# Performance work log

Hardware: AMD Instinct MI355X
Metric: run time of the kernel (lower is better)

Reference implementation:

```python
import jax, jax.numpy as jnp
import numpy as np

CENTER_LR = 0.5  # EMA learning rate for centers (init arg lr)


def setup_inputs() -> dict:
    key = jax.random.key(0)
    k1, k2, k3 = jax.random.split(key, 3)
    B, D, C = 131072, 256, 1000
    feats = jax.random.normal(k1, (B, D), dtype=jnp.float32)
    centers = jax.random.normal(k2, (C, D), dtype=jnp.float32)
    labels = jax.random.randint(k3, (B,), 0, C, dtype=jnp.int64)
    return {"feats": feats, "centers": centers, "labels": labels}


def reference(feats, centers, labels):
    # EMA center update (done under no_grad in the original):
    # for each class c present in the batch:
    #   centers[c] = (1-lr)*centers[c] + lr*mean(feats[labels==c])
    C = centers.shape[0]
    counts = jax.ops.segment_sum(jnp.ones(labels.shape, feats.dtype), labels,
                                 num_segments=C)                       # [C]
    sums = jax.ops.segment_sum(feats, labels, num_segments=C)          # [C, D]
    means = sums / jnp.maximum(counts, 1.0)[:, None]                   # [C, D]
    present = (counts > 0)[:, None]
    new_centers = jnp.where(present,
                            (1.0 - CENTER_LR) * centers + CENTER_LR * means,
                            centers)                                   # [C, D]
    new_centers = jax.lax.stop_gradient(new_centers)
    # loss = 0.5 * mean_i ||f_i - c_{y_i}||^2
    sel = new_centers[labels]                                          # [B, D]
    diff = feats - sel
    loss = 0.5 * jnp.mean(jnp.sum(diff * diff, axis=1))
    return loss
```

## Files before the change

kernel.cpp:

```cpp
#include <hip/hip_runtime.h>


#define DDIM 256
#define DDIM4 64
#define CHUNK 2048

__global__ __launch_bounds__(1024) void k0_zero(int* __restrict__ counts,
                                                float* __restrict__ scalars) {
    int t = threadIdx.x;
    counts[t] = 0;
    if (t < 4) scalars[t] = 0.f;
}

__global__ __launch_bounds__(256) void k1_hist(const int* __restrict__ labels,
                                               int* __restrict__ counts,
                                               int B, int C) {
    __shared__ int h[1024];
    for (int i = threadIdx.x; i < 1024; i += 256) h[i] = 0;
    __syncthreads();
    int stride = gridDim.x * 256;
    for (int i = blockIdx.x * 256 + threadIdx.x; i < B; i += stride)
        atomicAdd(&h[labels[i]], 1);
    __syncthreads();
    for (int i = threadIdx.x; i < C; i += 256) {
        int v = h[i];
        if (v) atomicAdd(&counts[i], v);
    }
}

__global__ __launch_bounds__(1024) void k2_scan(const int* __restrict__ counts,
                                                int* __restrict__ offsets,
                                                int* __restrict__ cursor, int C) {
    __shared__ int sc[1024];
    int t = threadIdx.x;
    int mine = (t < C) ? counts[t] : 0;
    sc[t] = mine;
    __syncthreads();
    for (int off = 1; off < 1024; off <<= 1) {
        int add = (t >= off) ? sc[t - off] : 0;
        __syncthreads();
        sc[t] += add;
        __syncthreads();
    }
    if (t < C) {
        int e = sc[t] - mine;
        offsets[t] = e;
        cursor[t]  = e;
    }
}

__global__ __launch_bounds__(256) void k3_scatter(const int* __restrict__ labels,
                                                  int* __restrict__ cursor,
                                                  int* __restrict__ rowidx, int B) {
    int stride = gridDim.x * 256;
    for (int i = blockIdx.x * 256 + threadIdx.x; i < B; i += stride) {
        int c = labels[i];
        int pos = atomicAdd(&cursor[c], 1);
        rowidx[pos] = i;
    }
}

__global__ __launch_bounds__(256) void k4_class(const float4* __restrict__ feats4,
                                                const float* __restrict__ centers,
                                                const int* __restrict__ rowidx,
                                                const int* __restrict__ counts,
                                                const int* __restrict__ offsets,
                                                float* __restrict__ scalars) {
    __shared__ int rows[CHUNK];
    __shared__ float comb[4 * DDIM];
    __shared__ float red[12];

    int c = blockIdx.x;
    int count = counts[c];
    int start = offsets[c];
    int t = threadIdx.x;
    int wave = t >> 6, lane = t & 63;

    float4 acc = make_float4(0.f, 0.f, 0.f, 0.f);
    float ff = 0.f;

    for (int cs = 0; cs < count; cs += CHUNK) {
        int n = min(CHUNK, count - cs);
        for (int i = t; i < n; i += 256) rows[i] = rowidx[start + cs + i];
        __syncthreads();
        int r = wave;
        for (; r + 12 < n; r += 16) {
            int r0 = rows[r], r1 = rows[r + 4], r2 = rows[r + 8], r3 = rows[r + 12];
            float4 v0 = feats4[r0 * DDIM4 + lane];
            float4 v1 = feats4[r1 * DDIM4 + lane];
            float4 v2 = feats4[r2 * DDIM4 + lane];
            float4 v3 = feats4[r3 * DDIM4 + lane];
            acc.x += v0.x; acc.y += v0.y; acc.z += v0.z; acc.w += v0.w;
            ff += v0.x*v0.x + v0.y*v0.y + v0.z*v0.z + v0.w*v0.w;
            acc.x += v1.x; acc.y += v1.y; acc.z += v1.z; acc.w += v1.w;
            ff += v1.x*v1.x + v1.y*v1.y + v1.z*v1.z + v1.w*v1.w;
            acc.x += v2.x; acc.y += v2.y; acc.z += v2.z; acc.w += v2.w;
            ff += v2.x*v2.x + v2.y*v2.y + v2.z*v2.z + v2.w*v2.w;
            acc.x += v3.x; acc.y += v3.y; acc.z += v3.z; acc.w += v3.w;
            ff += v3.x*v3.x + v3.y*v3.y + v3.z*v3.z + v3.w*v3.w;
        }
        for (; r < n; r += 4) {
            float4 v = feats4[rows[r] * DDIM4 + lane];
            acc.x += v.x; acc.y += v.y; acc.z += v.z; acc.w += v.w;
            ff += v.x*v.x + v.y*v.y + v.z*v.z + v.w*v.w;
        }
        __syncthreads();
    }

    comb[wave * DDIM + lane * 4 + 0] = acc.x;
    comb[wave * DDIM + lane * 4 + 1] = acc.y;
    comb[wave * DDIM + lane * 4 + 2] = acc.z;
    comb[wave * DDIM + lane * 4 + 3] = acc.w;
    __syncthreads();

    int d = t;
    float s  = comb[d] + comb[DDIM + d] + comb[2 * DDIM + d] + comb[3 * DDIM + d];
    float co = centers[c * DDIM + d];
    float nc = (count > 0) ? 0.5f * co + 0.5f * s / (float)count : co;
    float dotv = nc * s;
    float ccv  = nc * nc * (float)count;

#pragma unroll
    for (int off = 32; off > 0; off >>= 1) {
        ff   += __shfl_down(ff, off);
        dotv += __shfl_down(dotv, off);
        ccv  += __shfl_down(ccv, off);
    }
    if (lane == 0) {
        red[wave * 3 + 0] = ff;
        red[wave * 3 + 1] = dotv;
        red[wave * 3 + 2] = ccv;
    }
    __syncthreads();
    if (t == 0) {
        float a = red[0] + red[3] + red[6] + red[9];
        float b = red[1] + red[4] + red[7] + red[10];
        float e = red[2] + red[5] + red[8] + red[11];
        atomicAdd(&scalars[0], a);
        atomicAdd(&scalars[1], b);
        atomicAdd(&scalars[2], e);
    }
}

__global__ void k5_final(const float* __restrict__ scalars, float* __restrict__ out, int B) {
    if (threadIdx.x == 0 && blockIdx.x == 0) {
        out[0] = 0.5f / (float)B * (scalars[0] - 2.f * scalars[1] + scalars[2]);
    }
}

extern "C" void kernel_launch(void* const* d_in, const int* in_sizes, int n_in,
                              void* d_out, int out_size, void* d_ws, size_t ws_size,
                              hipStream_t stream) {
    const float* feats   = (const float*)d_in[0];
    const float* centers = (const float*)d_in[1];
    const int*   labels  = (const int*)d_in[2];

    int B = in_sizes[2];
    int Dv = in_sizes[0] / B;
    int C = in_sizes[1] / Dv;
    (void)Dv; (void)n_in; (void)ws_size;

    int* W = (int*)d_ws;
    int* counts  = W;
    int* offsets = W + 1024;
    int* cursor  = W + 2048;
    float* scalars = (float*)(W + 3072);
    int* rowidx  = W + 3072 + 16;

    k0_zero<<<1, 1024, 0, stream>>>(counts, scalars);
    k1_hist<<<256, 256, 0, stream>>>(labels, counts, B, C);
    k2_scan<<<1, 1024, 0, stream>>>(counts, offsets, cursor, C);
    int sblocks = (B + 255) / 256;
    if (sblocks > 512) sblocks = 512;
    k3_scatter<<<sblocks, 256, 0, stream>>>(labels, cursor, rowidx, B);
    k4_class<<<C, 256, 0, stream>>>((const float4*)feats, centers, rowidx,
                                    counts, offsets, scalars);
    k5_final<<<1, 64, 0, stream>>>(scalars, (float*)d_out, B);
}
```

Measured before the change: 103.6 us.

## Split per-class gather into four segments with atomic partial sums and separate epilogue

The per-class reduction kernel now launches four blocks per class, each summing a quarter of that class's rows and atomically adding its partial sums into a zeroed workspace buffer. A new epilogue kernel then computes the EMA-updated centers and the dot and norm terms from those sums. The aim is more parallelism and better load balance across the GPU, since 1000 blocks of about 131 rows each may underfill the device. In exchange it adds global float atomics, a larger zeroing pass and an extra kernel launch.

```diff
diff --git a/kernel.cpp b/kernel.cpp
--- a/kernel.cpp
+++ b/kernel.cpp
@@ -3,13 +3,13 @@
 
 #define DDIM 256
 #define DDIM4 64
-#define CHUNK 2048
+#define SEGS 4
+#define CHUNK 1024
 
-__global__ __launch_bounds__(1024) void k0_zero(int* __restrict__ counts,
-                                                float* __restrict__ scalars) {
-    int t = threadIdx.x;
-    counts[t] = 0;
-    if (t < 4) scalars[t] = 0.f;
+__global__ __launch_bounds__(256) void k0_zero(int4* __restrict__ p, int n4) {
+    int stride = gridDim.x * 256;
+    int4 z = make_int4(0, 0, 0, 0);
+    for (int i = blockIdx.x * 256 + threadIdx.x; i < n4; i += stride) p[i] = z;
 }
 
 __global__ __launch_bounds__(256) void k1_hist(const int* __restrict__ labels,
@@ -60,31 +60,37 @@
     }
 }
 
-__global__ __launch_bounds__(256) void k4_class(const float4* __restrict__ feats4,
-                                                const float* __restrict__ centers,
-                                                const int* __restrict__ rowidx,
-                                                const int* __restrict__ counts,
-                                                const int* __restrict__ offsets,
-                                                float* __restrict__ scalars) {
+__global__ __launch_bounds__(256) void k4_gather(const float4* __restrict__ feats4,
+                                                 const int* __restrict__ rowidx,
+                                                 const int* __restrict__ counts,
+                                                 const int* __restrict__ offsets,
+                                                 float* __restrict__ sums,
+                                                 float* __restrict__ scalars) {
     __shared__ int rows[CHUNK];
     __shared__ float comb[4 * DDIM];
-    __shared__ float red[12];
+    __shared__ float redf[4];
 
-    int c = blockIdx.x;
+    int c = blockIdx.x >> 2;
+    int s = blockIdx.x & 3;
     int count = counts[c];
-    int start = offsets[c];
+    int seg = (count + SEGS - 1) >> 2;
+    int s0 = s * seg;
+    int n = min(seg, count - s0);
+    if (n <= 0) return;
+    int start = offsets[c] + s0;
+
     int t = threadIdx.x;
     int wave = t >> 6, lane = t & 63;
 
     float4 acc = make_float4(0.f, 0.f, 0.f, 0.f);
     float ff = 0.f;
 
-    for (int cs = 0; cs < count; cs += CHUNK) {
-        int n = min(CHUNK, count - cs);
-        for (int i = t; i < n; i += 256) rows[i] = rowidx[start + cs + i];
+    for (int cs = 0; cs < n; cs += CHUNK) {
+        int m = min(CHUNK, n - cs);
+        for (int i = t; i < m; i += 256) rows[i] = rowidx[start + cs + i];
         __syncthreads();
         int r = wave;
-        for (; r + 12 < n; r += 16) {
+        for (; r + 12 < m; r += 16) {
             int r0 = rows[r], r1 = rows[r + 4], r2 = rows[r + 8], r3 = rows[r + 12];
             float4 v0 = feats4[r0 * DDIM4 + lane];
             float4 v1 = feats4[r1 * DDIM4 + lane];
@@ -99,7 +105,7 @@
             acc.x += v3.x; acc.y += v3.y; acc.z += v3.z; acc.w += v3.w;
             ff += v3.x*v3.x + v3.y*v3.y + v3.z*v3.z + v3.w*v3.w;
         }
-        for (; r < n; r += 4) {
+        for (; r < m; r += 4) {
             float4 v = feats4[rows[r] * DDIM4 + lane];
             acc.x += v.x; acc.y += v.y; acc.z += v.z; acc.w += v.w;
             ff += v.x*v.x + v.y*v.y + v.z*v.z + v.w*v.w;
@@ -113,36 +119,46 @@
     comb[wave * DDIM + lane * 4 + 3] = acc.w;
     __syncthreads();
 
-    int d = t;
-    float s  = comb[d] + comb[DDIM + d] + comb[2 * DDIM + d] + comb[3 * DDIM + d];
-    float co = centers[c * DDIM + d];
+    float v = comb[t] + comb[DDIM + t] + comb[2 * DDIM + t] + comb[3 * DDIM + t];
+    atomicAdd(&sums[c * DDIM + t], v);
+
+#pragma unroll
+    for (int off = 32; off > 0; off >>= 1) ff += __shfl_down(ff, off);
+    if (lane == 0) redf[wave] = ff;
+    __syncthreads();
+    if (t == 0) atomicAdd(&scalars[0], redf[0] + redf[1] + redf[2] + redf[3]);
+}
+
+__global__ __launch_bounds__(256) void k5_epilogue(const float* __restrict__ sums,
+                                                   const float* __restrict__ centers,
+                                                   const int* __restrict__ counts,
+                                                   float* __restrict__ scalars) {
+    __shared__ float red[8];
+    int c = blockIdx.x;
+    int t = threadIdx.x;
+    int wave = t >> 6, lane = t & 63;
+    int count = counts[c];
+
+    float s  = sums[c * DDIM + t];
+    float co = centers[c * DDIM + t];
     float nc = (count > 0) ? 0.5f * co + 0.5f * s / (float)count : co;
     float dotv = nc * s;
     float ccv  = nc * nc * (float)count;
 
 #pragma unroll
     for (int off = 32; off > 0; off >>= 1) {
-        ff   += __shfl_down(ff, off);
         dotv += __shfl_down(dotv, off);
         ccv  += __shfl_down(ccv, off);
     }
-    if (lane == 0) {
-        red[wave * 3 + 0] = ff;
-        red[wave * 3 + 1] = dotv;
-        red[wave * 3 + 2] = ccv;
-    }
+    if (lane == 0) { red[wave * 2 + 0] = dotv; red[wave * 2 + 1] = ccv; }
     __syncthreads();
     if (t == 0) {
-        float a = red[0] + red[3] + red[6] + red[9];
-        float b = red[1] + red[4] + red[7] + red[10];
-        float e = red[2] + red[5] + red[8] + red[11];
-        atomicAdd(&scalars[0], a);
-        atomicAdd(&scalars[1], b);
-        atomicAdd(&scalars[2], e);
+        atomicAdd(&scalars[1], red[0] + red[2] + red[4] + red[6]);
+        atomicAdd(&scalars[2], red[1] + red[3] + red[5] + red[7]);
     }
 }
 
-__global__ void k5_final(const float* __restrict__ scalars, float* __restrict__ out, int B) {
+__global__ void k6_final(const float* __restrict__ scalars, float* __restrict__ out, int B) {
     if (threadIdx.x == 0 && blockIdx.x == 0) {
         out[0] = 0.5f / (float)B * (scalars[0] - 2.f * scalars[1] + scalars[2]);
     }
@@ -161,19 +177,22 @@
     (void)Dv; (void)n_in; (void)ws_size;
 
     int* W = (int*)d_ws;
-    int* counts  = W;
-    int* offsets = W + 1024;
-    int* cursor  = W + 2048;
-    float* scalars = (float*)(W + 3072);
-    int* rowidx  = W + 3072 + 16;
+    int* counts    = W;
+    float* scalars = (float*)(W + 1024);
+    float* sums    = (float*)(W + 1040);
+    int* offsets   = W + 1040 + C * DDIM;
+    int* cursor    = offsets + 1024;
+    int* rowidx    = cursor + 1024;
 
-    k0_zero<<<1, 1024, 0, stream>>>(counts, scalars);
+    int zero_ints = 1040 + C * DDIM;
+    k0_zero<<<256, 256, 0, stream>>>((int4*)W, zero_ints / 4);
     k1_hist<<<256, 256, 0, stream>>>(labels, counts, B, C);
     k2_scan<<<1, 1024, 0, stream>>>(counts, offsets, cursor, C);
     int sblocks = (B + 255) / 256;
     if (sblocks > 512) sblocks = 512;
     k3_scatter<<<sblocks, 256, 0, stream>>>(labels, cursor, rowidx, B);
-    k4_class<<<C, 256, 0, stream>>>((const float4*)feats, centers, rowidx,
-                                    counts, offsets, scalars);
-    k5_final<<<1, 64, 0, stream>>>(scalars, (float*)d_out, B);
+    k4_gather<<<C * SEGS, 256, 0, stream>>>((const float4*)feats, rowidx,
+                                            counts, offsets, sums, scalars);
+    k5_epilogue<<<C, 256, 0, stream>>>(sums, centers, counts, scalars);
+    k6_final<<<1, 64, 0, stream>>>(scalars, (float*)d_out, B);
 }
```

Measured after the change: 137.4 us. 32.7% more time.
